# Kernel tuning notes

Measured on AMD Instinct MI355X. Metric: run time of the kernel, lower is better.

The kernel has to match this reference:

```python
import jax, jax.numpy as jnp
import numpy as np

B, S, DM, DA, H, F = 4, 1024, 512, 512, 8, 16
D = DA // H  # per-head depth = 64


def setup_inputs() -> dict:
    key = jax.random.key(0)
    ks = jax.random.split(key, 10)
    w = lambda i, shape: jax.random.normal(ks[i], shape, jnp.float32) * 0.02
    return {
        "q": jax.random.normal(ks[0], (B, S, DM), jnp.float32),
        "k": jax.random.normal(ks[1], (B, S, DM), jnp.float32),
        "v": jax.random.normal(ks[2], (B, S, DM), jnp.float32),
        "xdiff": jax.random.normal(ks[3], (B, S, S, F), jnp.float32),
        "Wq": w(4, (DM, DA)), "bq": jnp.zeros((DA,), jnp.float32),
        "Wk": w(5, (DM, DA)), "bk": jnp.zeros((DA,), jnp.float32),
        "Wv": w(6, (DM, DA)), "bv": jnp.zeros((DA,), jnp.float32),
        "Wx": w(7, (DA, H * F)), "bx": jnp.zeros((H * F,), jnp.float32),
        "Wo": w(8, (DA, DM)), "bo": jnp.zeros((DM,), jnp.float32),
    }


def reference(q, k, v, xdiff, Wq, bq, Wk, bk, Wv, bv, Wx, bx, Wo, bo):
    b, s, _ = q.shape
    qp = q @ Wq + bq                      # [B,S,DA]
    kp = k @ Wk + bk                      # [B,S,DA]
    vp = v @ Wv + bv                      # [B,S,DA]
    x = qp @ Wx + bx                      # [B,S,H*F]  (note: wx applied to projected q)
    qh = qp.reshape(b, s, H, D).transpose(0, 2, 1, 3)   # [B,H,S,D]
    kh = kp.reshape(b, s, H, D).transpose(0, 2, 1, 3)
    vh = vp.reshape(b, s, H, D).transpose(0, 2, 1, 3)
    xh = x.reshape(b, s, H, F)                           # [B,S,H,F]
    # xdiff relative bias: matmul(xdiff, x^T) then transpose -> [B,H,Sq,Sk]
    x_logits = jnp.einsum('bqkf,bqhf->bhqk', xdiff, xh)
    scaled_x_logits = 2.0 * x_logits / jnp.sqrt(jnp.float32(F))
    logits = jnp.einsum('bhqd,bhkd->bhqk', qh, kh) / jnp.sqrt(jnp.float32(D))
    logits = logits + scaled_x_logits
    attn = jax.nn.softmax(logits, axis=-1)               # [B,H,Sq,Sk]
    out = jnp.einsum('bhqk,bhkd->bhqd', attn, vh)        # [B,H,S,D]
    out = out.transpose(0, 2, 1, 3).reshape(b, s, DA)    # [B,S,DA]
    output = out @ Wo + bo                               # [B,S,DM]
    return (output, attn)
```

## Files before the change

kernel.cpp:

```cpp
#include <hip/hip_runtime.h>

typedef unsigned int uint;
typedef unsigned short ushort;
typedef __attribute__((ext_vector_type(4))) float f32x4;
typedef __attribute__((ext_vector_type(8))) __bf16 bf16x8;

#define MFMA16(a,b,c) __builtin_amdgcn_mfma_f32_16x16x32_bf16(a,b,c,0,0,0)

__device__ __forceinline__ ushort f2bf(float f){
  uint u = __float_as_uint(f);
  u += 0x7fffu + ((u>>16)&1u);
  return (ushort)(u>>16);
}
__device__ __forceinline__ float bf2f(ushort s){ return __uint_as_float(((uint)s)<<16); }
__device__ __forceinline__ uint packbf2(float a, float b){ return (uint)f2bf(a) | ((uint)f2bf(b)<<16); }

__global__ __launch_bounds__(256) void wt_kernel(const float* __restrict__ W,
    ushort* __restrict__ WT, int K, int N){
  __shared__ uint tile[64*65];
  const int k0 = blockIdx.y<<6, n0 = blockIdx.x<<6;
  const int tid = threadIdx.x;
  {
    const int row = tid>>4, c4 = (tid&15)<<2;
    #pragma unroll
    for (int i=0;i<4;++i){
      int r = row + (i<<4);
      float4 v = *reinterpret_cast<const float4*>(W + (size_t)(k0+r)*N + n0 + c4);
      tile[r*65 + c4    ] = f2bf(v.x);
      tile[r*65 + c4 + 1] = f2bf(v.y);
      tile[r*65 + c4 + 2] = f2bf(v.z);
      tile[r*65 + c4 + 3] = f2bf(v.w);
    }
  }
  __syncthreads();
  {
    const int n = tid>>3, k8 = (tid&7)<<3;
    #pragma unroll
    for (int j=0;j<2;++j){
      int nn = n + (j<<5);
      ushort t0=(ushort)tile[(k8+0)*65+nn], t1=(ushort)tile[(k8+1)*65+nn];
      ushort t2=(ushort)tile[(k8+2)*65+nn], t3=(ushort)tile[(k8+3)*65+nn];
      ushort t4=(ushort)tile[(k8+4)*65+nn], t5=(ushort)tile[(k8+5)*65+nn];
      ushort t6=(ushort)tile[(k8+6)*65+nn], t7=(ushort)tile[(k8+7)*65+nn];
      uint4 pk = make_uint4((uint)t0|((uint)t1<<16), (uint)t2|((uint)t3<<16),
                            (uint)t4|((uint)t5<<16), (uint)t6|((uint)t7<<16));
      *reinterpret_cast<uint4*>(WT + (size_t)(n0+nn)*K + k0 + k8) = pk;
    }
  }
}

template<bool A_F32, bool OUT_F32>
__global__ __launch_bounds__(256) void gemm_bt(const void* __restrict__ Av,
    const ushort* __restrict__ Bt, const float* __restrict__ bias,
    void* __restrict__ Cv, int M, int N, int K){
  __shared__ ushort As[64*48];
  __shared__ ushort Bs[64*48];
  const int tid = threadIdx.x;
  const int m0 = blockIdx.y<<6, n0 = blockIdx.x<<6;
  const int wave = tid>>6, lane = tid&63;
  const int wr = wave&1, wc = wave>>1;
  const int fl = lane&15, quad = lane>>4;
  f32x4 acc[2][2] = {};
  const int srow = tid>>2, sk = (tid&3)<<3;
  for (int k0 = 0; k0 < K; k0 += 32){
    if (A_F32){
      const float* A = (const float*)Av;
      const float4* pa = reinterpret_cast<const float4*>(A + (size_t)(m0+srow)*K + k0 + sk);
      float4 v0 = pa[0], v1 = pa[1];
      uint4 pk = make_uint4(packbf2(v0.x,v0.y), packbf2(v0.z,v0.w),
                            packbf2(v1.x,v1.y), packbf2(v1.z,v1.w));
      *reinterpret_cast<uint4*>(&As[srow*48 + sk]) = pk;
    } else {
      const ushort* A = (const ushort*)Av;
      *reinterpret_cast<uint4*>(&As[srow*48 + sk]) =
          *reinterpret_cast<const uint4*>(A + (size_t)(m0+srow)*K + k0 + sk);
    }
    *reinterpret_cast<uint4*>(&Bs[srow*48 + sk]) =
        *reinterpret_cast<const uint4*>(Bt + (size_t)(n0+srow)*K + k0 + sk);
    __syncthreads();
    bf16x8 a0 = *reinterpret_cast<const bf16x8*>(&As[(32*wr      + fl)*48 + quad*8]);
    bf16x8 a1 = *reinterpret_cast<const bf16x8*>(&As[(32*wr + 16 + fl)*48 + quad*8]);
    bf16x8 b0 = *reinterpret_cast<const bf16x8*>(&Bs[(32*wc      + fl)*48 + quad*8]);
    bf16x8 b1 = *reinterpret_cast<const bf16x8*>(&Bs[(32*wc + 16 + fl)*48 + quad*8]);
    acc[0][0] = MFMA16(a0,b0,acc[0][0]);
    acc[0][1] = MFMA16(a0,b1,acc[0][1]);
    acc[1][0] = MFMA16(a1,b0,acc[1][0]);
    acc[1][1] = MFMA16(a1,b1,acc[1][1]);
    __syncthreads();
  }
  #pragma unroll
  for (int t=0;t<2;++t)
  #pragma unroll
  for (int u=0;u<2;++u){
    #pragma unroll
    for (int r=0;r<4;++r){
      int row = m0 + 32*wr + 16*t + quad*4 + r;
      int col = n0 + 32*wc + 16*u + fl;
      float vv = acc[t][u][r] + bias[col];
      if (OUT_F32) ((float*)Cv)[(size_t)row*N + col] = vv;
      else         ((ushort*)Cv)[(size_t)row*N + col] = f2bf(vv);
    }
  }
}

__global__ __launch_bounds__(256) void vtrans(const ushort* __restrict__ vp,
    ushort* __restrict__ vT){
  __shared__ ushort tile[64*72];
  const int bh = blockIdx.y;
  const int b = bh>>3, h = bh&7;
  const int k0 = blockIdx.x<<6;
  const int tid = threadIdx.x;
  #pragma unroll
  for (int i=0;i<2;++i){
    int c = tid + (i<<8);
    int row = c>>3, ch = (c&7)<<3;
    uint4 v = *reinterpret_cast<const uint4*>(
        vp + ((size_t)(b*1024 + k0 + row)<<9) + (h<<6) + ch);
    *reinterpret_cast<uint4*>(&tile[row*72 + ch]) = v;
  }
  __syncthreads();
  #pragma unroll
  for (int i=0;i<2;++i){
    int c = tid + (i<<8);
    int d = c>>3, sc = (c&7)<<3;
    ushort t0 = tile[(sc+0)*72 + d], t1 = tile[(sc+1)*72 + d];
    ushort t2 = tile[(sc+2)*72 + d], t3 = tile[(sc+3)*72 + d];
    ushort t4 = tile[(sc+4)*72 + d], t5 = tile[(sc+5)*72 + d];
    ushort t6 = tile[(sc+6)*72 + d], t7 = tile[(sc+7)*72 + d];
    uint4 pk = make_uint4((uint)t0|((uint)t1<<16), (uint)t2|((uint)t3<<16),
                          (uint)t4|((uint)t5<<16), (uint)t6|((uint)t7<<16));
    *reinterpret_cast<uint4*>(vT + (((size_t)bh<<6) + d)*1024 + k0 + sc) = pk;
  }
}

__global__ __launch_bounds__(256) void xl_kernel(const float* __restrict__ xdiff,
    const ushort* __restrict__ xb, ushort* __restrict__ xl){
  const int bq = blockIdx.x;
  const int b = bq>>10, q = bq&1023;
  __shared__ float sx[8][16];
  const int tid = threadIdx.x;
  if (tid < 128) sx[tid>>4][tid&15] = bf2f(xb[(size_t)bq*128 + tid]);
  __syncthreads();
  const float* xd = xdiff + (size_t)bq*16384;
  #pragma unroll
  for (int i=0;i<4;++i){
    int k = tid + (i<<8);
    const float4* p = reinterpret_cast<const float4*>(xd + (size_t)k*16);
    float4 v0 = p[0], v1 = p[1], v2 = p[2], v3 = p[3];
    #pragma unroll
    for (int h=0; h<8; ++h){
      const float4* s = reinterpret_cast<const float4*>(&sx[h][0]);
      float4 s0=s[0], s1=s[1], s2=s[2], s3=s[3];
      float a = v0.x*s0.x + v0.y*s0.y + v0.z*s0.z + v0.w*s0.w
              + v1.x*s1.x + v1.y*s1.y + v1.z*s1.z + v1.w*s1.w
              + v2.x*s2.x + v2.y*s2.y + v2.z*s2.z + v2.w*s2.w
              + v3.x*s3.x + v3.y*s3.y + v3.z*s3.z + v3.w*s3.w;
      xl[(((size_t)((b<<3)+h)<<10) + q)*1024 + k] = f2bf(0.5f*a);
    }
  }
}

__global__ __launch_bounds__(512) void attn_kernel(const ushort* __restrict__ qp,
    const ushort* __restrict__ kp, const ushort* __restrict__ vT,
    const ushort* __restrict__ xl, float* __restrict__ attn, ushort* __restrict__ outc){
  __shared__ ushort s_p[32*1024];
  const int qt = blockIdx.x, h = blockIdx.y, b = blockIdx.z;
  const int q0 = qt<<5;
  const int tid = threadIdx.x, lane = tid&63, wave = tid>>6;
  const int wr = wave&1, wc = wave>>1;
  const int fl = lane&15, quad = lane>>4;
  const size_t bS = (size_t)b<<10;
  const int bh = (b<<3) + h;

  bf16x8 aq[2];
  #pragma unroll
  for (int s=0;s<2;++s)
    aq[s] = *reinterpret_cast<const bf16x8*>(
        qp + ((bS + q0 + (wr<<4) + fl)<<9) + (h<<6) + (s<<5) + (quad<<3));

  for (int kt=0; kt<16; ++kt){
    f32x4 acc = {};
    #pragma unroll
    for (int s=0;s<2;++s){
      bf16x8 bf = *reinterpret_cast<const bf16x8*>(
          kp + ((bS + (kt<<6) + (wc<<4) + fl)<<9) + (h<<6) + (s<<5) + (quad<<3));
      acc = MFMA16(aq[s], bf, acc);
    }
    #pragma unroll
    for (int r=0;r<4;++r){
      int row = (wr<<4) + (quad<<2) + r;
      int col = (kt<<6) + (wc<<4) + fl;
      int chunk = (col>>3) ^ ((row>>1)&7);
      s_p[(row<<10) + (chunk<<3) + (col&7)] = f2bf(acc[r]*0.125f);
    }
  }
  __syncthreads();

  const int r = tid>>4, seg = tid&15, swz = (r>>1)&7;
  const ushort* xrow = xl + (((size_t)bh<<10) + q0 + r)*1024;
  float* arow = attn + (((size_t)bh<<10) + q0 + r)*1024;
  float mx = -3.0e38f;
  for (int cc=0; cc<8; ++cc){
    int chunk = (cc<<4) + seg;
    uint4 lv = *reinterpret_cast<uint4*>(&s_p[(r<<10) + ((chunk^swz)<<3)]);
    uint4 xv = *reinterpret_cast<const uint4*>(xrow + (chunk<<3));
    float f0 = bf2f(lv.x&0xffff)+bf2f(xv.x&0xffff), f1 = bf2f(lv.x>>16)+bf2f(xv.x>>16);
    float f2 = bf2f(lv.y&0xffff)+bf2f(xv.y&0xffff), f3 = bf2f(lv.y>>16)+bf2f(xv.y>>16);
    float f4 = bf2f(lv.z&0xffff)+bf2f(xv.z&0xffff), f5 = bf2f(lv.z>>16)+bf2f(xv.z>>16);
    float f6 = bf2f(lv.w&0xffff)+bf2f(xv.w&0xffff), f7 = bf2f(lv.w>>16)+bf2f(xv.w>>16);
    mx = fmaxf(mx, fmaxf(fmaxf(fmaxf(f0,f1),fmaxf(f2,f3)), fmaxf(fmaxf(f4,f5),fmaxf(f6,f7))));
    uint4 pk = make_uint4(packbf2(f0,f1), packbf2(f2,f3), packbf2(f4,f5), packbf2(f6,f7));
    *reinterpret_cast<uint4*>(&s_p[(r<<10) + ((chunk^swz)<<3)]) = pk;
  }
  #pragma unroll
  for (int d=1; d<16; d<<=1) mx = fmaxf(mx, __shfl_xor(mx, d));
  float sum = 0.f;
  for (int cc=0; cc<8; ++cc){
    int chunk = (cc<<4) + seg;
    uint4 lv = *reinterpret_cast<uint4*>(&s_p[(r<<10) + ((chunk^swz)<<3)]);
    ushort u0 = f2bf(__expf(bf2f(lv.x&0xffff)-mx)), u1 = f2bf(__expf(bf2f(lv.x>>16)-mx));
    ushort u2 = f2bf(__expf(bf2f(lv.y&0xffff)-mx)), u3 = f2bf(__expf(bf2f(lv.y>>16)-mx));
    ushort u4 = f2bf(__expf(bf2f(lv.z&0xffff)-mx)), u5 = f2bf(__expf(bf2f(lv.z>>16)-mx));
    ushort u6 = f2bf(__expf(bf2f(lv.w&0xffff)-mx)), u7 = f2bf(__expf(bf2f(lv.w>>16)-mx));
    sum += bf2f(u0)+bf2f(u1)+bf2f(u2)+bf2f(u3)+bf2f(u4)+bf2f(u5)+bf2f(u6)+bf2f(u7);
    uint4 pk = make_uint4((uint)u0|((uint)u1<<16), (uint)u2|((uint)u3<<16),
                          (uint)u4|((uint)u5<<16), (uint)u6|((uint)u7<<16));
    *reinterpret_cast<uint4*>(&s_p[(r<<10) + ((chunk^swz)<<3)]) = pk;
  }
  #pragma unroll
  for (int d=1; d<16; d<<=1) sum += __shfl_xor(sum, d);
  float inv = 1.f/sum;
  for (int cc=0; cc<8; ++cc){
    int chunk = (cc<<4) + seg;
    uint4 lv = *reinterpret_cast<uint4*>(&s_p[(r<<10) + ((chunk^swz)<<3)]);
    float o0 = bf2f(lv.x&0xffff)*inv, o1 = bf2f(lv.x>>16)*inv;
    float o2 = bf2f(lv.y&0xffff)*inv, o3 = bf2f(lv.y>>16)*inv;
    float o4 = bf2f(lv.z&0xffff)*inv, o5 = bf2f(lv.z>>16)*inv;
    float o6 = bf2f(lv.w&0xffff)*inv, o7 = bf2f(lv.w>>16)*inv;
    *reinterpret_cast<float4*>(arow + (chunk<<3))     = make_float4(o0,o1,o2,o3);
    *reinterpret_cast<float4*>(arow + (chunk<<3) + 4) = make_float4(o4,o5,o6,o7);
    uint4 pk = make_uint4(packbf2(o0,o1), packbf2(o2,o3), packbf2(o4,o5), packbf2(o6,o7));
    *reinterpret_cast<uint4*>(&s_p[(r<<10) + ((chunk^swz)<<3)]) = pk;
  }
  __syncthreads();

  f32x4 o = {};
  const int ar = (wr<<4) + fl;
  const int aswz = (ar>>1)&7;
  for (int kt=0; kt<16; ++kt){
    #pragma unroll
    for (int s=0;s<2;++s){
      int chunk = (kt<<3) + (s<<2) + quad;
      bf16x8 af = *reinterpret_cast<const bf16x8*>(&s_p[(ar<<10) + ((chunk^aswz)<<3)]);
      bf16x8 bf = *reinterpret_cast<const bf16x8*>(
          vT + (((size_t)bh<<6) + (wc<<4) + fl)*1024 + (kt<<6) + (s<<5) + (quad<<3));
      o = MFMA16(af, bf, o);
    }
  }
  #pragma unroll
  for (int r4=0;r4<4;++r4){
    int row = (wr<<4) + (quad<<2) + r4;
    int col = (wc<<4) + fl;
    outc[((bS + q0 + row)<<9) + (h<<6) + col] = f2bf(o[r4]);
  }
}

extern "C" void kernel_launch(void* const* d_in, const int* in_sizes, int n_in,
                              void* d_out, int out_size, void* d_ws, size_t ws_size,
                              hipStream_t stream){
  (void)in_sizes; (void)n_in; (void)out_size; (void)ws_size;
  const float* q  = (const float*)d_in[0];
  const float* k  = (const float*)d_in[1];
  const float* v  = (const float*)d_in[2];
  const float* xd = (const float*)d_in[3];
  const float* Wq = (const float*)d_in[4];  const float* bq = (const float*)d_in[5];
  const float* Wk = (const float*)d_in[6];  const float* bk = (const float*)d_in[7];
  const float* Wv = (const float*)d_in[8];  const float* bv = (const float*)d_in[9];
  const float* Wx = (const float*)d_in[10]; const float* bx = (const float*)d_in[11];
  const float* Wo = (const float*)d_in[12]; const float* bo = (const float*)d_in[13];
  char* ws = (char*)d_ws;
  const size_t MB = 1u<<20;
  ushort* qp  = (ushort*)(ws);
  ushort* kp  = (ushort*)(ws + 4*MB);
  ushort* vp  = (ushort*)(ws + 8*MB);
  ushort* vT  = (ushort*)(ws + 12*MB);
  ushort* xb  = (ushort*)(ws + 16*MB);
  ushort* xl  = (ushort*)(ws + 17*MB);
  ushort* oc  = (ushort*)(ws + 81*MB);
  ushort* WqT = (ushort*)(ws + 85*MB);
  ushort* WkT = (ushort*)(ws + 85*MB + 1*524288);
  ushort* WvT = (ushort*)(ws + 85*MB + 2*524288);
  ushort* WoT = (ushort*)(ws + 85*MB + 3*524288);
  ushort* WxT = (ushort*)(ws + 85*MB + 4*524288);
  float* out0 = (float*)d_out;
  float* attn = (float*)d_out + 2097152;

  wt_kernel<<<dim3(8,8), 256, 0, stream>>>(Wq, WqT, 512, 512);
  wt_kernel<<<dim3(8,8), 256, 0, stream>>>(Wk, WkT, 512, 512);
  wt_kernel<<<dim3(8,8), 256, 0, stream>>>(Wv, WvT, 512, 512);
  wt_kernel<<<dim3(8,8), 256, 0, stream>>>(Wo, WoT, 512, 512);
  wt_kernel<<<dim3(2,8), 256, 0, stream>>>(Wx, WxT, 512, 128);

  gemm_bt<true,false><<<dim3(8,64), 256, 0, stream>>>(q, WqT, bq, qp, 4096, 512, 512);
  gemm_bt<true,false><<<dim3(8,64), 256, 0, stream>>>(k, WkT, bk, kp, 4096, 512, 512);
  gemm_bt<true,false><<<dim3(8,64), 256, 0, stream>>>(v, WvT, bv, vp, 4096, 512, 512);
  gemm_bt<false,false><<<dim3(2,64), 256, 0, stream>>>(qp, WxT, bx, xb, 4096, 128, 512);

  vtrans<<<dim3(16,32), 256, 0, stream>>>(vp, vT);
  xl_kernel<<<4096, 256, 0, stream>>>(xd, xb, xl);
  attn_kernel<<<dim3(32,8,4), 512, 0, stream>>>(qp, kp, vT, xl, attn, oc);
  gemm_bt<false,true><<<dim3(8,64), 256, 0, stream>>>(oc, WoT, bo, out0, 4096, 512, 512);
}
```

Before: 614.3 us.

## Batch weight transposes and QKV GEMMs, prefetch GEMM tiles, keep softmax in registers

```diff
diff --git a/kernel.cpp b/kernel.cpp
--- a/kernel.cpp
+++ b/kernel.cpp
@@ -3,6 +3,7 @@
 typedef unsigned int uint;
 typedef unsigned short ushort;
 typedef __attribute__((ext_vector_type(4))) float f32x4;
+typedef __attribute__((ext_vector_type(4))) uint u32x4;
 typedef __attribute__((ext_vector_type(8))) __bf16 bf16x8;
 
 #define MFMA16(a,b,c) __builtin_amdgcn_mfma_f32_16x16x32_bf16(a,b,c,0,0,0)
@@ -15,10 +16,16 @@
 __device__ __forceinline__ float bf2f(ushort s){ return __uint_as_float(((uint)s)<<16); }
 __device__ __forceinline__ uint packbf2(float a, float b){ return (uint)f2bf(a) | ((uint)f2bf(b)<<16); }
 
-__global__ __launch_bounds__(256) void wt_kernel(const float* __restrict__ W,
-    ushort* __restrict__ WT, int K, int N){
+struct WtArgs { const float* W[5]; ushort* T[5]; int K[5]; int N[5]; };
+
+__global__ __launch_bounds__(256) void wt_kernel(WtArgs args){
   __shared__ uint tile[64*65];
+  const int z = blockIdx.z;
+  const float* __restrict__ W = args.W[z];
+  ushort* __restrict__ WT = args.T[z];
+  const int K = args.K[z], N = args.N[z];
   const int k0 = blockIdx.y<<6, n0 = blockIdx.x<<6;
+  if (n0 >= N || k0 >= K) return;
   const int tid = threadIdx.x;
   {
     const int row = tid>>4, c4 = (tid&15)<<2;
@@ -50,11 +57,9 @@
 }
 
 template<bool A_F32, bool OUT_F32>
-__global__ __launch_bounds__(256) void gemm_bt(const void* __restrict__ Av,
-    const ushort* __restrict__ Bt, const float* __restrict__ bias,
-    void* __restrict__ Cv, int M, int N, int K){
-  __shared__ ushort As[64*48];
-  __shared__ ushort Bs[64*48];
+__device__ __forceinline__ void gemm_body(ushort* As, ushort* Bs,
+    const void* __restrict__ Av, const ushort* __restrict__ Bt,
+    const float* __restrict__ bias, void* __restrict__ Cv, int M, int N, int K){
   const int tid = threadIdx.x;
   const int m0 = blockIdx.y<<6, n0 = blockIdx.x<<6;
   const int wave = tid>>6, lane = tid&63;
@@ -62,22 +67,34 @@
   const int fl = lane&15, quad = lane>>4;
   f32x4 acc[2][2] = {};
   const int srow = tid>>2, sk = (tid&3)<<3;
+  float4 va0, va1; uint4 ua; uint4 ub;
+  if (A_F32){
+    const float4* pa = reinterpret_cast<const float4*>((const float*)Av + (size_t)(m0+srow)*K + sk);
+    va0 = pa[0]; va1 = pa[1];
+  } else {
+    ua = *reinterpret_cast<const uint4*>((const ushort*)Av + (size_t)(m0+srow)*K + sk);
+  }
+  ub = *reinterpret_cast<const uint4*>(Bt + (size_t)(n0+srow)*K + sk);
   for (int k0 = 0; k0 < K; k0 += 32){
     if (A_F32){
-      const float* A = (const float*)Av;
-      const float4* pa = reinterpret_cast<const float4*>(A + (size_t)(m0+srow)*K + k0 + sk);
-      float4 v0 = pa[0], v1 = pa[1];
-      uint4 pk = make_uint4(packbf2(v0.x,v0.y), packbf2(v0.z,v0.w),
-                            packbf2(v1.x,v1.y), packbf2(v1.z,v1.w));
-      *reinterpret_cast<uint4*>(&As[srow*48 + sk]) = pk;
+      *reinterpret_cast<uint4*>(&As[srow*48 + sk]) = make_uint4(
+          packbf2(va0.x,va0.y), packbf2(va0.z,va0.w),
+          packbf2(va1.x,va1.y), packbf2(va1.z,va1.w));
     } else {
-      const ushort* A = (const ushort*)Av;
-      *reinterpret_cast<uint4*>(&As[srow*48 + sk]) =
-          *reinterpret_cast<const uint4*>(A + (size_t)(m0+srow)*K + k0 + sk);
-    }
-    *reinterpret_cast<uint4*>(&Bs[srow*48 + sk]) =
-        *reinterpret_cast<const uint4*>(Bt + (size_t)(n0+srow)*K + k0 + sk);
+      *reinterpret_cast<uint4*>(&As[srow*48 + sk]) = ua;
+    }
+    *reinterpret_cast<uint4*>(&Bs[srow*48 + sk]) = ub;
     __syncthreads();
+    const int kn = k0 + 32;
+    if (kn < K){
+      if (A_F32){
+        const float4* pa = reinterpret_cast<const float4*>((const float*)Av + (size_t)(m0+srow)*K + kn + sk);
+        va0 = pa[0]; va1 = pa[1];
+      } else {
+        ua = *reinterpret_cast<const uint4*>((const ushort*)Av + (size_t)(m0+srow)*K + kn + sk);
+      }
+      ub = *reinterpret_cast<const uint4*>(Bt + (size_t)(n0+srow)*K + kn + sk);
+    }
     bf16x8 a0 = *reinterpret_cast<const bf16x8*>(&As[(32*wr      + fl)*48 + quad*8]);
     bf16x8 a1 = *reinterpret_cast<const bf16x8*>(&As[(32*wr + 16 + fl)*48 + quad*8]);
     bf16x8 b0 = *reinterpret_cast<const bf16x8*>(&Bs[(32*wc      + fl)*48 + quad*8]);
@@ -101,6 +118,30 @@
       else         ((ushort*)Cv)[(size_t)row*N + col] = f2bf(vv);
     }
   }
+}
+
+template<bool A_F32, bool OUT_F32>
+__global__ __launch_bounds__(256) void gemm_bt(const void* __restrict__ Av,
+    const ushort* __restrict__ Bt, const float* __restrict__ bias,
+    void* __restrict__ Cv, int M, int N, int K){
+  __shared__ ushort As[64*48];
+  __shared__ ushort Bs[64*48];
+  gemm_body<A_F32,OUT_F32>(As, Bs, Av, Bt, bias, Cv, M, N, K);
+}
+
+__global__ __launch_bounds__(256) void gemm3_kernel(
+    const float* A0, const float* A1, const float* A2,
+    const ushort* T0, const ushort* T1, const ushort* T2,
+    const float* b0, const float* b1, const float* b2,
+    ushort* C0, ushort* C1, ushort* C2, int M, int N, int K){
+  __shared__ ushort As[64*48];
+  __shared__ ushort Bs[64*48];
+  const int z = blockIdx.z;
+  const float* A = z==0 ? A0 : (z==1 ? A1 : A2);
+  const ushort* Bt = z==0 ? T0 : (z==1 ? T1 : T2);
+  const float* bi = z==0 ? b0 : (z==1 ? b1 : b2);
+  ushort* C = z==0 ? C0 : (z==1 ? C1 : C2);
+  gemm_body<true,false>(As, Bs, A, Bt, bi, C, M, N, K);
 }
 
 __global__ __launch_bounds__(256) void vtrans(const ushort* __restrict__ vp,
@@ -142,25 +183,31 @@
   if (tid < 128) sx[tid>>4][tid&15] = bf2f(xb[(size_t)bq*128 + tid]);
   __syncthreads();
   const float* xd = xdiff + (size_t)bq*16384;
+  f32x4 v[4][4];
   #pragma unroll
   for (int i=0;i<4;++i){
     int k = tid + (i<<8);
-    const float4* p = reinterpret_cast<const float4*>(xd + (size_t)k*16);
-    float4 v0 = p[0], v1 = p[1], v2 = p[2], v3 = p[3];
-    #pragma unroll
-    for (int h=0; h<8; ++h){
-      const float4* s = reinterpret_cast<const float4*>(&sx[h][0]);
-      float4 s0=s[0], s1=s[1], s2=s[2], s3=s[3];
-      float a = v0.x*s0.x + v0.y*s0.y + v0.z*s0.z + v0.w*s0.w
-              + v1.x*s1.x + v1.y*s1.y + v1.z*s1.z + v1.w*s1.w
-              + v2.x*s2.x + v2.y*s2.y + v2.z*s2.z + v2.w*s2.w
-              + v3.x*s3.x + v3.y*s3.y + v3.z*s3.z + v3.w*s3.w;
+    const f32x4* p = reinterpret_cast<const f32x4*>(xd + (size_t)k*16);
+    #pragma unroll
+    for (int j=0;j<4;++j) v[i][j] = __builtin_nontemporal_load(p + j);
+  }
+  #pragma unroll
+  for (int h=0; h<8; ++h){
+    const float4* s = reinterpret_cast<const float4*>(&sx[h][0]);
+    float4 s0=s[0], s1=s[1], s2=s[2], s3=s[3];
+    #pragma unroll
+    for (int i=0;i<4;++i){
+      int k = tid + (i<<8);
+      float a = v[i][0].x*s0.x + v[i][0].y*s0.y + v[i][0].z*s0.z + v[i][0].w*s0.w
+              + v[i][1].x*s1.x + v[i][1].y*s1.y + v[i][1].z*s1.z + v[i][1].w*s1.w
+              + v[i][2].x*s2.x + v[i][2].y*s2.y + v[i][2].z*s2.z + v[i][2].w*s2.w
+              + v[i][3].x*s3.x + v[i][3].y*s3.y + v[i][3].z*s3.z + v[i][3].w*s3.w;
       xl[(((size_t)((b<<3)+h)<<10) + q)*1024 + k] = f2bf(0.5f*a);
     }
   }
 }
 
-__global__ __launch_bounds__(512) void attn_kernel(const ushort* __restrict__ qp,
+__global__ __launch_bounds__(512,4) void attn_kernel(const ushort* __restrict__ qp,
     const ushort* __restrict__ kp, const ushort* __restrict__ vT,
     const ushort* __restrict__ xl, float* __restrict__ attn, ushort* __restrict__ outc){
   __shared__ ushort s_p[32*1024];
@@ -178,13 +225,14 @@
     aq[s] = *reinterpret_cast<const bf16x8*>(
         qp + ((bS + q0 + (wr<<4) + fl)<<9) + (h<<6) + (s<<5) + (quad<<3));
 
+  #pragma unroll 4
   for (int kt=0; kt<16; ++kt){
     f32x4 acc = {};
     #pragma unroll
     for (int s=0;s<2;++s){
-      bf16x8 bf = *reinterpret_cast<const bf16x8*>(
+      bf16x8 bfr = *reinterpret_cast<const bf16x8*>(
           kp + ((bS + (kt<<6) + (wc<<4) + fl)<<9) + (h<<6) + (s<<5) + (quad<<3));
-      acc = MFMA16(aq[s], bf, acc);
+      acc = MFMA16(aq[s], bfr, acc);
     }
     #pragma unroll
     for (int r=0;r<4;++r){
@@ -199,62 +247,67 @@
   const int r = tid>>4, seg = tid&15, swz = (r>>1)&7;
   const ushort* xrow = xl + (((size_t)bh<<10) + q0 + r)*1024;
   float* arow = attn + (((size_t)bh<<10) + q0 + r)*1024;
+  uint4 rg[8];
   float mx = -3.0e38f;
+  #pragma unroll
   for (int cc=0; cc<8; ++cc){
     int chunk = (cc<<4) + seg;
     uint4 lv = *reinterpret_cast<uint4*>(&s_p[(r<<10) + ((chunk^swz)<<3)]);
-    uint4 xv = *reinterpret_cast<const uint4*>(xrow + (chunk<<3));
+    u32x4 xv = __builtin_nontemporal_load(
+        reinterpret_cast<const u32x4*>(xrow + (chunk<<3)));
     float f0 = bf2f(lv.x&0xffff)+bf2f(xv.x&0xffff), f1 = bf2f(lv.x>>16)+bf2f(xv.x>>16);
     float f2 = bf2f(lv.y&0xffff)+bf2f(xv.y&0xffff), f3 = bf2f(lv.y>>16)+bf2f(xv.y>>16);
     float f4 = bf2f(lv.z&0xffff)+bf2f(xv.z&0xffff), f5 = bf2f(lv.z>>16)+bf2f(xv.z>>16);
     float f6 = bf2f(lv.w&0xffff)+bf2f(xv.w&0xffff), f7 = bf2f(lv.w>>16)+bf2f(xv.w>>16);
     mx = fmaxf(mx, fmaxf(fmaxf(fmaxf(f0,f1),fmaxf(f2,f3)), fmaxf(fmaxf(f4,f5),fmaxf(f6,f7))));
-    uint4 pk = make_uint4(packbf2(f0,f1), packbf2(f2,f3), packbf2(f4,f5), packbf2(f6,f7));
-    *reinterpret_cast<uint4*>(&s_p[(r<<10) + ((chunk^swz)<<3)]) = pk;
+    rg[cc] = make_uint4(packbf2(f0,f1), packbf2(f2,f3), packbf2(f4,f5), packbf2(f6,f7));
   }
   #pragma unroll
   for (int d=1; d<16; d<<=1) mx = fmaxf(mx, __shfl_xor(mx, d));
   float sum = 0.f;
+  #pragma unroll
   for (int cc=0; cc<8; ++cc){
-    int chunk = (cc<<4) + seg;
-    uint4 lv = *reinterpret_cast<uint4*>(&s_p[(r<<10) + ((chunk^swz)<<3)]);
+    uint4 lv = rg[cc];
     ushort u0 = f2bf(__expf(bf2f(lv.x&0xffff)-mx)), u1 = f2bf(__expf(bf2f(lv.x>>16)-mx));
     ushort u2 = f2bf(__expf(bf2f(lv.y&0xffff)-mx)), u3 = f2bf(__expf(bf2f(lv.y>>16)-mx));
     ushort u4 = f2bf(__expf(bf2f(lv.z&0xffff)-mx)), u5 = f2bf(__expf(bf2f(lv.z>>16)-mx));
     ushort u6 = f2bf(__expf(bf2f(lv.w&0xffff)-mx)), u7 = f2bf(__expf(bf2f(lv.w>>16)-mx));
     sum += bf2f(u0)+bf2f(u1)+bf2f(u2)+bf2f(u3)+bf2f(u4)+bf2f(u5)+bf2f(u6)+bf2f(u7);
-    uint4 pk = make_uint4((uint)u0|((uint)u1<<16), (uint)u2|((uint)u3<<16),
-                          (uint)u4|((uint)u5<<16), (uint)u6|((uint)u7<<16));
-    *reinterpret_cast<uint4*>(&s_p[(r<<10) + ((chunk^swz)<<3)]) = pk;
+    rg[cc] = make_uint4((uint)u0|((uint)u1<<16), (uint)u2|((uint)u3<<16),
+                        (uint)u4|((uint)u5<<16), (uint)u6|((uint)u7<<16));
   }
   #pragma unroll
   for (int d=1; d<16; d<<=1) sum += __shfl_xor(sum, d);
   float inv = 1.f/sum;
+  #pragma unroll
   for (int cc=0; cc<8; ++cc){
     int chunk = (cc<<4) + seg;
-    uint4 lv = *reinterpret_cast<uint4*>(&s_p[(r<<10) + ((chunk^swz)<<3)]);
+    uint4 lv = rg[cc];
     float o0 = bf2f(lv.x&0xffff)*inv, o1 = bf2f(lv.x>>16)*inv;
     float o2 = bf2f(lv.y&0xffff)*inv, o3 = bf2f(lv.y>>16)*inv;
     float o4 = bf2f(lv.z&0xffff)*inv, o5 = bf2f(lv.z>>16)*inv;
     float o6 = bf2f(lv.w&0xffff)*inv, o7 = bf2f(lv.w>>16)*inv;
-    *reinterpret_cast<float4*>(arow + (chunk<<3))     = make_float4(o0,o1,o2,o3);
-    *reinterpret_cast<float4*>(arow + (chunk<<3) + 4) = make_float4(o4,o5,o6,o7);
-    uint4 pk = make_uint4(packbf2(o0,o1), packbf2(o2,o3), packbf2(o4,o5), packbf2(o6,o7));
-    *reinterpret_cast<uint4*>(&s_p[(r<<10) + ((chunk^swz)<<3)]) = pk;
+    __builtin_nontemporal_store(f32x4{o0,o1,o2,o3},
+        reinterpret_cast<f32x4*>(arow + (chunk<<3)));
+    __builtin_nontemporal_store(f32x4{o4,o5,o6,o7},
+        reinterpret_cast<f32x4*>(arow + (chunk<<3) + 4));
+    *reinterpret_cast<uint4*>(&s_p[(r<<10) + ((chunk^swz)<<3)]) =
+        make_uint4(packbf2(o0,o1), packbf2(o2,o3), packbf2(o4,o5), packbf2(o6,o7));
   }
   __syncthreads();
 
   f32x4 o = {};
   const int ar = (wr<<4) + fl;
   const int aswz = (ar>>1)&7;
+  #pragma unroll 2
   for (int kt=0; kt<16; ++kt){
     #pragma unroll
     for (int s=0;s<2;++s){
       int chunk = (kt<<3) + (s<<2) + quad;
       bf16x8 af = *reinterpret_cast<const bf16x8*>(&s_p[(ar<<10) + ((chunk^aswz)<<3)]);
-      bf16x8 bf = *reinterpret_cast<const bf16x8*>(
+      bf16x8 bfr = *reinterpret_cast<const bf16x8*>(
           vT + (((size_t)bh<<6) + (wc<<4) + fl)*1024 + (kt<<6) + (s<<5) + (quad<<3));
-      o = MFMA16(af, bf, o);
+      o = MFMA16(af, bfr, o);
     }
   }
   #pragma unroll
@@ -295,15 +348,15 @@
   float* out0 = (float*)d_out;
   float* attn = (float*)d_out + 2097152;
 
-  wt_kernel<<<dim3(8,8), 256, 0, stream>>>(Wq, WqT, 512, 512);
-  wt_kernel<<<dim3(8,8), 256, 0, stream>>>(Wk, WkT, 512, 512);
-  wt_kernel<<<dim3(8,8), 256, 0, stream>>>(Wv, WvT, 512, 512);
-  wt_kernel<<<dim3(8,8), 256, 0, stream>>>(Wo, WoT, 512, 512);
-  wt_kernel<<<dim3(2,8), 256, 0, stream>>>(Wx, WxT, 512, 128);
-
-  gemm_bt<true,false><<<dim3(8,64), 256, 0, stream>>>(q, WqT, bq, qp, 4096, 512, 512);
-  gemm_bt<true,false><<<dim3(8,64), 256, 0, stream>>>(k, WkT, bk, kp, 4096, 512, 512);
-  gemm_bt<true,false><<<dim3(8,64), 256, 0, stream>>>(v, WvT, bv, vp, 4096, 512, 512);
+  WtArgs wa;
+  wa.W[0]=Wq; wa.W[1]=Wk; wa.W[2]=Wv; wa.W[3]=Wo; wa.W[4]=Wx;
+  wa.T[0]=WqT; wa.T[1]=WkT; wa.T[2]=WvT; wa.T[3]=WoT; wa.T[4]=WxT;
+  wa.K[0]=512; wa.K[1]=512; wa.K[2]=512; wa.K[3]=512; wa.K[4]=512;
+  wa.N[0]=512; wa.N[1]=512; wa.N[2]=512; wa.N[3]=512; wa.N[4]=128;
+  wt_kernel<<<dim3(8,8,5), 256, 0, stream>>>(wa);
+
+  gemm3_kernel<<<dim3(8,64,3), 256, 0, stream>>>(q, k, v, WqT, WkT, WvT,
+                                                 bq, bk, bv, qp, kp, vp, 4096, 512, 512);
   gemm_bt<false,false><<<dim3(2,64), 256, 0, stream>>>(qp, WxT, bx, xb, 4096, 128, 512);
 
   vtrans<<<dim3(16,32), 256, 0, stream>>>(vp, vT);
```

Result: slower. 628.8 us (+2.4%).
